# Performance work log

Hardware: AMD Instinct MI355X
Metric: run time of the kernel (lower is better)

## Reference

```python
import jax, jax.numpy as jnp
import numpy as np

# MORRConfig_20um_MQ ring parameters
A = 0.8578   # attenuation factor a
R = 0.8985   # coupling factor r

IN_C, OUT_C, KS, STRIDE, PAD, MB = 32, 64, 3, 1, 1, 8
WIN = IN_C * KS * KS                      # 288 = kernel_size^2 * in_channel
WIN_PAD = ((WIN + MB - 1) // MB) * MB     # padded to multiple of miniblock
OUT_PAD = ((OUT_C + MB - 1) // MB) * MB
Q = WIN_PAD // MB                         # grid_dim_x = 36
P = OUT_PAD // MB                         # grid_dim_y = 8
MORR_GAIN = (100.0 / (WIN // MB)) ** 0.5  # input power normalization


def mrr_tr(phi):
    # all-pass MORR roundtrip-phase -> transmission intensity
    # T = (a^2 - 2ar cos(phi) + r^2) / (1 - 2ar cos(phi) + (ar)^2)
    c = 2.0 * A * R * jnp.cos(phi)
    return (A * A + R * R - c) / (1.0 + (A * R) ** 2 - c)


def im2col(x):
    # torch F.unfold ordering: feature dim ordered (C, ki, kj)
    B, C, H, W = x.shape
    xp = jnp.pad(x, ((0, 0), (0, 0), (PAD, PAD), (PAD, PAD)))
    Ho = (H + 2 * PAD - KS) // STRIDE + 1
    Wo = (W + 2 * PAD - KS) // STRIDE + 1
    cols = [xp[:, :, i:i + Ho * STRIDE:STRIDE, j:j + Wo * STRIDE:STRIDE]
            for i in range(KS) for j in range(KS)]
    p = jnp.stack(cols, axis=2)               # [B, C, KS*KS, Ho, Wo]
    return p.reshape(B, C * KS * KS, Ho * Wo), Ho, Wo


def setup_inputs() -> dict:
    key = jax.random.key(0)
    k1, k2, k3 = jax.random.split(key, 3)
    x = jax.random.uniform(k1, (8, IN_C, 64, 64), dtype=jnp.float32)  # intensity-encoded, nonneg
    weight = jax.random.uniform(k2, (P, Q, MB), dtype=jnp.float32) * 0.2  # nonneg MORR weights
    morr_output_scale = jax.random.normal(k3, (max(1, Q // 2) + 1,), dtype=jnp.float32) * 0.1
    return {"x": x, "weight": weight, "morr_output_scale": morr_output_scale}


def reference(x, weight, morr_output_scale):
    B = x.shape[0]
    cols, Ho, Wo = im2col(x)
    xb = cols.transpose(0, 2, 1)
    if WIN_PAD > WIN:
        xb = jnp.pad(xb, ((0, 0), (0, 0), (0, WIN_PAD - WIN)))
    xb = xb.reshape(-1, Q, MB)                # [Bs, Q, MB]
    inten = (xb * xb) * MORR_GAIN             # optical intensity (power-normalized)

    # block-circulant weighted phase accumulation == circular conv per (p,q) block, via rFFT
    Wf = jnp.fft.rfft(weight, axis=-1)        # [P, Q, MBf]
    Xf = jnp.fft.rfft(inten, axis=-1)         # [Bs, Q, MBf]
    phase = jnp.fft.irfft(Xf[:, None, :, :] * Wf[None], n=MB, axis=-1)  # [Bs, P, Q, MB]

    tr = mrr_tr(phase)                        # MORR nonlinear transfer

    # differential rails: learnable balancing factor per block-column pair (+1 pad scale)
    half = morr_output_scale[:-1]             # [Q//2]
    if Q % 2 == 0:
        scale = jnp.concatenate([half, -half])                              # [Q]
    else:
        scale = jnp.concatenate([half, morr_output_scale[-1:], -half])      # [Q]

    out = jnp.einsum("bpqk,q->bpk", tr, scale).reshape(-1, OUT_PAD)[:, :OUT_C]
    out = out.reshape(B, Ho * Wo, OUT_C).transpose(0, 2, 1).reshape(B, OUT_C, Ho, Wo)
    return out
```

## Files before the change

kernel.cpp:

```cpp
#include <hip/hip_runtime.h>

#define THREADS 256

#define IN_C 32
#define OUT_C 64
#define HW 64
#define Q_N 36
#define P_N 8
#define MB 8

__global__ __launch_bounds__(THREADS)
void morr_conv_kernel(const float* __restrict__ x,
                      const float* __restrict__ weight,
                      const float* __restrict__ mos,
                      float* __restrict__ out)
{
    __shared__ float sx[IN_C * 101];
    __shared__ float wlds[P_N * Q_N * MB];
    __shared__ float slds[Q_N];

    const int tid = threadIdx.x;
    const int blk = blockIdx.x;
    const int b    = blk >> 6;
    const int tile = blk & 63;
    const int ty = tile >> 3, tx = tile & 7;
    const int h0 = ty * 8, w0 = tx * 8;

    const float GAIN = 1.6666666666666667f;

    for (int idx = tid; idx < 3200; idx += THREADS) {
        int c   = idx / 100;
        int rem = idx - c * 100;
        int h   = rem / 10;
        int w   = rem - h * 10;
        int gh = h0 + h - 1;
        int gw = w0 + w - 1;
        float v = 0.f;
        if ((unsigned)gh < 64u && (unsigned)gw < 64u)
            v = x[((b * IN_C + c) * HW + gh) * HW + gw];
        sx[c * 101 + h * 10 + w] = GAIN * v * v;
    }
    for (int idx = tid; idx < P_N * Q_N * MB; idx += THREADS)
        wlds[idx] = weight[idx];
    if (tid < Q_N)
        slds[tid] = (tid < 18) ? mos[tid] : -mos[tid - 18];
    __syncthreads();

    const int pg  = tid & 3;
    const int pix = tid >> 2;
    const int px = pix & 7, py = pix >> 3;

    const float A_ = 0.8578f, R_ = 0.8985f;
    const float S_ = A_ * A_ + R_ * R_;
    const float D_ = 1.f + (A_ * R_) * (A_ * R_);
    const float C2 = 2.f * A_ * R_;

    float acc[16];
#pragma unroll
    for (int i = 0; i < 16; ++i) acc[i] = 0.f;

    const int dbase = py * 10 + px;

#pragma unroll 1
    for (int z = 0; z < 4; ++z) {
        const int sbase = (z * 8) * 101 + dbase;
        const int qz = z * 9;
#pragma unroll
        for (int qi = 0; qi < 9; ++qi) {
            float iv[8];
#pragma unroll
            for (int j = 0; j < 8; ++j) {
                const int u  = qi * 8 + j;
                const int cu = u / 9;
                const int r  = u - cu * 9;
                const int ki = r / 3;
                const int kj = r - ki * 3;
                iv[j] = sx[sbase + cu * 101 + ki * 10 + kj];
            }
            const float sc = slds[qz + qi];
#pragma unroll
            for (int pi = 0; pi < 2; ++pi) {
                const int p  = pg * 2 + pi;
                const int wb = p * (Q_N * MB) + (qz + qi) * MB;
                float wv[8];
#pragma unroll
                for (int m = 0; m < 8; ++m) wv[m] = wlds[wb + m];
                float ph[8];
#pragma unroll
                for (int k = 0; k < 8; ++k) ph[k] = 0.f;
#pragma unroll
                for (int j = 0; j < 8; ++j) {
#pragma unroll
                    for (int k = 0; k < 8; ++k) {
                        ph[k] = fmaf(iv[j], wv[(k - j) & 7], ph[k]);
                    }
                }
#pragma unroll
                for (int k = 0; k < 8; ++k) {
                    float c  = C2 * __cosf(ph[k]);
                    float tr = (S_ - c) * __builtin_amdgcn_rcpf(D_ - c);
                    acc[pi * 8 + k] = fmaf(sc, tr, acc[pi * 8 + k]);
                }
            }
        }
    }

    const int ho = h0 + py, wo = w0 + px;
    float* op = out + ((b * OUT_C + pg * 16) * HW + ho) * HW + wo;
#pragma unroll
    for (int pi = 0; pi < 2; ++pi) {
#pragma unroll
        for (int k = 0; k < 8; ++k) {
            op[(pi * 8 + k) * (HW * HW)] = acc[pi * 8 + k];
        }
    }
}

extern "C" void kernel_launch(void* const* d_in, const int* in_sizes, int n_in,
                              void* d_out, int out_size, void* d_ws, size_t ws_size,
                              hipStream_t stream) {
    const float* x      = (const float*)d_in[0];
    const float* weight = (const float*)d_in[1];
    const float* mos    = (const float*)d_in[2];
    float* out = (float*)d_out;

    dim3 grid(512), block(THREADS);
    hipLaunchKernelGGL(morr_conv_kernel, grid, block, 0, stream, x, weight, mos, out);
}
```

Measured before the change: 101.6 us.

## Simplify MORR transfer algebraically, use native cos, and retile to row strips

Rewrites the transmission as 1 + E/(D - c). Because the differential scale vector sums to zero, the constant term cancels, so only the reciprocal is accumulated and the result is scaled by E once at the end. Switches to the hardware cos builtin, which takes its argument in revolutions, so the weights are pre-scaled by 1/(2*pi) while staging. Retiles the work as one thread per pixel per output block over 32-wide row strips, with 1024 blocks and a launch-bounds occupancy hint. It also stores the weights q-major so each thread reads them with two float4 LDS loads. The trade-off is more halo staging per output pixel and less per-thread work to hide latency.

```diff
diff --git a/kernel.cpp b/kernel.cpp
--- a/kernel.cpp
+++ b/kernel.cpp
@@ -9,61 +9,70 @@
 #define P_N 8
 #define MB 8
 
-__global__ __launch_bounds__(THREADS)
+#define SXPLANE 102
+#define W2SZ (Q_N * P_N * MB)
+
+__global__ __launch_bounds__(THREADS, 4)
 void morr_conv_kernel(const float* __restrict__ x,
                       const float* __restrict__ weight,
                       const float* __restrict__ mos,
                       float* __restrict__ out)
 {
-    __shared__ float sx[IN_C * 101];
-    __shared__ float wlds[P_N * Q_N * MB];
+    __shared__ float sx[IN_C * SXPLANE];
+    __shared__ float w2[W2SZ];
     __shared__ float slds[Q_N];
 
     const int tid = threadIdx.x;
     const int blk = blockIdx.x;
-    const int b    = blk >> 6;
-    const int tile = blk & 63;
-    const int ty = tile >> 3, tx = tile & 7;
-    const int h0 = ty * 8, w0 = tx * 8;
+    const int b   = blk >> 7;
+    const int tile = blk & 127;
+    const int row = tile >> 1;
+    const int w0  = (tile & 1) << 5;
 
-    const float GAIN = 1.6666666666666667f;
+    const float GAIN    = 1.6666666666666667f;
+    const float INV2PI  = 0.15915494309189535f;
 
-    for (int idx = tid; idx < 3200; idx += THREADS) {
-        int c   = idx / 100;
-        int rem = idx - c * 100;
-        int h   = rem / 10;
-        int w   = rem - h * 10;
-        int gh = h0 + h - 1;
-        int gw = w0 + w - 1;
+    for (int idx = tid; idx < IN_C * SXPLANE; idx += THREADS) {
+        int c   = idx / SXPLANE;
+        int rem = idx - c * SXPLANE;
+        int r   = rem / 34;
+        int col = rem - r * 34;
+        int gh = row + r - 1;
+        int gw = w0 + col - 1;
         float v = 0.f;
         if ((unsigned)gh < 64u && (unsigned)gw < 64u)
             v = x[((b * IN_C + c) * HW + gh) * HW + gw];
-        sx[c * 101 + h * 10 + w] = GAIN * v * v;
+        sx[idx] = GAIN * v * v;
     }
-    for (int idx = tid; idx < P_N * Q_N * MB; idx += THREADS)
-        wlds[idx] = weight[idx];
+    for (int idx = tid; idx < W2SZ; idx += THREADS) {
+        int p   = idx / (Q_N * MB);
+        int rem = idx - p * (Q_N * MB);
+        int q   = rem >> 3;
+        int m   = idx & 7;
+        w2[(q * P_N + p) * MB + m] = weight[idx] * INV2PI;
+    }
     if (tid < Q_N)
         slds[tid] = (tid < 18) ? mos[tid] : -mos[tid - 18];
     __syncthreads();
 
-    const int pg  = tid & 3;
-    const int pix = tid >> 2;
-    const int px = pix & 7, py = pix >> 3;
+    const int px = tid & 31;
+    const int p  = tid >> 5;
 
     const float A_ = 0.8578f, R_ = 0.8985f;
     const float S_ = A_ * A_ + R_ * R_;
     const float D_ = 1.f + (A_ * R_) * (A_ * R_);
     const float C2 = 2.f * A_ * R_;
+    const float E_ = S_ - D_;
 
-    float acc[16];
+    float acc[8];
 #pragma unroll
-    for (int i = 0; i < 16; ++i) acc[i] = 0.f;
+    for (int i = 0; i < 8; ++i) acc[i] = 0.f;
 
-    const int dbase = py * 10 + px;
+    const float4* w4 = (const float4*)w2;
 
 #pragma unroll 1
     for (int z = 0; z < 4; ++z) {
-        const int sbase = (z * 8) * 101 + dbase;
+        const int sbase = (z * 8) * SXPLANE + px;
         const int qz = z * 9;
 #pragma unroll
         for (int qi = 0; qi < 9; ++qi) {
@@ -75,45 +84,36 @@
                 const int r  = u - cu * 9;
                 const int ki = r / 3;
                 const int kj = r - ki * 3;
-                iv[j] = sx[sbase + cu * 101 + ki * 10 + kj];
+                iv[j] = sx[sbase + cu * SXPLANE + ki * 34 + kj];
             }
             const float sc = slds[qz + qi];
+            const int wq = ((qz + qi) * P_N + p) * 2;
+            float4 wlo = w4[wq], whi = w4[wq + 1];
+            float wv[8] = {wlo.x, wlo.y, wlo.z, wlo.w, whi.x, whi.y, whi.z, whi.w};
+
+            float ph[8];
 #pragma unroll
-            for (int pi = 0; pi < 2; ++pi) {
-                const int p  = pg * 2 + pi;
-                const int wb = p * (Q_N * MB) + (qz + qi) * MB;
-                float wv[8];
+            for (int k = 0; k < 8; ++k) ph[k] = iv[0] * wv[k];
 #pragma unroll
-                for (int m = 0; m < 8; ++m) wv[m] = wlds[wb + m];
-                float ph[8];
+            for (int j = 1; j < 8; ++j) {
 #pragma unroll
-                for (int k = 0; k < 8; ++k) ph[k] = 0.f;
+                for (int k = 0; k < 8; ++k)
+                    ph[k] = fmaf(iv[j], wv[(k - j) & 7], ph[k]);
+            }
 #pragma unroll
-                for (int j = 0; j < 8; ++j) {
-#pragma unroll
-                    for (int k = 0; k < 8; ++k) {
-                        ph[k] = fmaf(iv[j], wv[(k - j) & 7], ph[k]);
-                    }
-                }
-#pragma unroll
-                for (int k = 0; k < 8; ++k) {
-                    float c  = C2 * __cosf(ph[k]);
-                    float tr = (S_ - c) * __builtin_amdgcn_rcpf(D_ - c);
-                    acc[pi * 8 + k] = fmaf(sc, tr, acc[pi * 8 + k]);
-                }
+            for (int k = 0; k < 8; ++k) {
+                float cc = __builtin_amdgcn_cosf(ph[k]);
+                float d  = fmaf(-C2, cc, D_);
+                float r_ = __builtin_amdgcn_rcpf(d);
+                acc[k] = fmaf(sc, r_, acc[k]);
             }
         }
     }
 
-    const int ho = h0 + py, wo = w0 + px;
-    float* op = out + ((b * OUT_C + pg * 16) * HW + ho) * HW + wo;
+    float* op = out + ((b * OUT_C + p * MB) * (HW * HW)) + row * HW + w0 + px;
 #pragma unroll
-    for (int pi = 0; pi < 2; ++pi) {
-#pragma unroll
-        for (int k = 0; k < 8; ++k) {
-            op[(pi * 8 + k) * (HW * HW)] = acc[pi * 8 + k];
-        }
-    }
+    for (int k = 0; k < 8; ++k)
+        op[k * (HW * HW)] = E_ * acc[k];
 }
 
 extern "C" void kernel_launch(void* const* d_in, const int* in_sizes, int n_in,
@@ -124,6 +124,6 @@
     const float* mos    = (const float*)d_in[2];
     float* out = (float*)d_out;
 
-    dim3 grid(512), block(THREADS);
+    dim3 grid(1024), block(THREADS);
     hipLaunchKernelGGL(morr_conv_kernel, grid, block, 0, stream, x, weight, mos, out);
 }
```

After: 96.11 us. 1.06x faster.
